# Optimization experiments

Hardware: AMD Instinct MI355X
Metric: run time of the kernel (lower is better)

Reference implementation:

```python
import jax, jax.numpy as jnp
import numpy as np

EPS_SLOPE = 1e-4
EPS_AVG = 1e-8
MIN_AVG = 1e-6
EPS_SCALE = 1e-3


def _slopes_yk(xk, delta_raw):
    # xk: [D, K] sorted knot x-positions; delta_raw: [D, K-1]
    seg_dx = xk[:, 1:] - xk[:, :-1]                      # [D, K-1]
    slopes = jax.nn.softplus(delta_raw) + EPS_SLOPE       # [D, K-1]
    avg = (slopes * seg_dx).sum(1, keepdims=True) / (seg_dx.sum(1, keepdims=True) + EPS_AVG)
    avg = jnp.maximum(avg, MIN_AVG)
    slopes = slopes / avg
    yk = jnp.concatenate(
        [jnp.zeros((xk.shape[0], 1), dtype=xk.dtype), jnp.cumsum(slopes * seg_dx, axis=1)],
        axis=1,
    )                                                     # [D, K]
    return slopes, yk


def setup_inputs() -> dict:
    key = jax.random.key(0)
    k1, k2, k3, k4, k5 = jax.random.split(key, 5)
    N, D, K = 1_000_000, 64, 32
    x = jax.random.normal(k1, (N, D), dtype=jnp.float32)
    # sorted knots per dim, spanning roughly the data range
    xk = jnp.sort(jax.random.normal(k2, (D, K), dtype=jnp.float32) * 2.0, axis=1)
    delta_raw = jax.random.normal(k3, (D, K - 1), dtype=jnp.float32) * 0.1
    scale_raw = jax.random.normal(k4, (D,), dtype=jnp.float32) * 0.1
    shift = jax.random.normal(k5, (D,), dtype=jnp.float32) * 0.1
    return {"x": x, "xk": xk, "delta_raw": delta_raw, "scale_raw": scale_raw, "shift": shift}


def reference(x, xk, delta_raw, scale_raw, shift):
    # x: [N, D]; xk: [D, K]
    D, K = xk.shape
    slopes, yk = _slopes_yk(xk, delta_raw)
    xT = x.T                                              # [D, N]
    # per-dim binary search (torch.searchsorted default == side='left')
    idx = jax.vmap(lambda knots, vals: jnp.searchsorted(knots, vals))(xk, xT)
    i0 = jnp.clip(idx, 1, K - 1) - 1                      # [D, N]
    x0 = jnp.take_along_axis(xk, i0, axis=1)              # [D, N]
    y0 = jnp.take_along_axis(yk, i0, axis=1)
    m = jnp.take_along_axis(slopes, i0, axis=1)
    y = (y0 + m * (xT - x0)).T                            # [N, D]
    scale = jax.nn.softplus(scale_raw) + EPS_SCALE
    return y * scale + shift
```

## Files before the change

kernel.cpp:

```cpp
#include <hip/hip_runtime.h>
#include <math.h>

#define D 64
#define KNOTS 32
#define NSEG 31
#define G 512
#define TPAD 516
#define SPAD 33

typedef float f4v __attribute__((ext_vector_type(4)));

__device__ __forceinline__ float softplus_f(float v) {
  return fmaxf(v, 0.f) + log1pf(expf(-fabsf(v)));
}

__global__ __launch_bounds__(512, 4) void pwl_fused(
    const float* __restrict__ x, const float* __restrict__ xk,
    const float* __restrict__ delta_raw, const float* __restrict__ scale_raw,
    const float* __restrict__ shift, float* __restrict__ out, int nrows) {
  __shared__ float kL[KNOTS * D];
  __shared__ float sA[D * SPAD];
  __shared__ float sB[D * SPAD];
  __shared__ unsigned char tab[D * TPAD];
  __shared__ float invS[D], nloS[D];

  const int tid = threadIdx.x;

  for (int i = tid; i < D * KNOTS; i += blockDim.x) {
    int d = i >> 5, j = i & 31;
    int sd = (d >> 2) | ((d & 3) << 4);
    kL[j * D + sd] = xk[i];
  }
  __syncthreads();

  if (tid < D) {
    const int sd = tid;
    const int d = ((sd & 15) << 2) | (sd >> 4);
    float num = 0.f, den = 0.f;
    for (int s = 0; s < NSEG; ++s) {
      float sp = softplus_f(delta_raw[d * NSEG + s]) + 1e-4f;
      float dx = kL[(s + 1) * D + sd] - kL[s * D + sd];
      num += sp * dx;
      den += dx;
    }
    float avg = fmaxf(num / (den + 1e-8f), 1e-6f);
    float scale = softplus_f(scale_raw[d]) + 1e-3f;
    float sh = shift[d];
    float y = 0.f;
    for (int s = 0; s < NSEG; ++s) {
      float sp = softplus_f(delta_raw[d * NSEG + s]) + 1e-4f;
      float m = sp / avg;
      float k0 = kL[s * D + sd];
      sA[sd * SPAD + s] = m * scale;
      sB[sd * SPAD + s] = (y - m * k0) * scale + sh;
      y += m * (kL[(s + 1) * D + sd] - k0);
    }
    float lo = kL[1 * D + sd];
    float hi = kL[(KNOTS - 1) * D + sd];
    float inv = (float)G / (hi - lo);
    invS[sd] = inv;
    nloS[sd] = -lo * inv;
  }
  __syncthreads();

  for (int p = tid; p < G * D; p += blockDim.x) {
    const int sd = p & 63;
    const int c = p >> 6;
    const float inv = invS[sd], nlo = nloS[sd];
    int b = 0;
#pragma unroll
    for (int half = 16; half > 0; half >>= 1) {
      float kv = kL[(b + half) * D + sd];
      float cf = fminf(fmaxf(fmaf(kv, inv, nlo), 0.f), (float)(G - 1));
      b += ((int)cf < c) ? half : 0;
    }
    tab[sd * TPAD + c] = (unsigned char)min(b, 30);
  }
  __syncthreads();

  const int lane = tid & 63;
  const int q = lane & 15;
  const int sd0 = q, sd1 = q + 16, sd2 = q + 32, sd3 = q + 48;
  const float inv0 = invS[sd0], nlo0 = nloS[sd0];
  const float inv1 = invS[sd1], nlo1 = nloS[sd1];
  const float inv2 = invS[sd2], nlo2 = nloS[sd2];
  const float inv3 = invS[sd3], nlo3 = nloS[sd3];

  const float* xp = x;
  float* op = out;
  const f4v* __restrict__ x4 = (const f4v*)x;
  f4v* __restrict__ o4 = (f4v*)out;

  auto evalquad = [&](f4v xv) -> f4v {
    float cf0 = fminf(fmaxf(fmaf(xv.x, inv0, nlo0), 0.f), (float)(G - 1));
    float cf1 = fminf(fmaxf(fmaf(xv.y, inv1, nlo1), 0.f), (float)(G - 1));
    float cf2 = fminf(fmaxf(fmaf(xv.z, inv2, nlo2), 0.f), (float)(G - 1));
    float cf3 = fminf(fmaxf(fmaf(xv.w, inv3, nlo3), 0.f), (float)(G - 1));
    int i0 = tab[sd0 * TPAD + (int)cf0];
    int i1 = tab[sd1 * TPAD + (int)cf1];
    int i2 = tab[sd2 * TPAD + (int)cf2];
    int i3 = tab[sd3 * TPAD + (int)cf3];
    f4v r;
    r.x = fmaf(sA[sd0 * SPAD + i0], xv.x, sB[sd0 * SPAD + i0]);
    r.y = fmaf(sA[sd1 * SPAD + i1], xv.y, sB[sd1 * SPAD + i1]);
    r.z = fmaf(sA[sd2 * SPAD + i2], xv.z, sB[sd2 * SPAD + i2]);
    r.w = fmaf(sA[sd3 * SPAD + i3], xv.w, sB[sd3 * SPAD + i3]);
    return r;
  };

  const int wid = (int)(blockIdx.x * blockDim.x + tid) >> 6;
  const int nw = (int)(gridDim.x * blockDim.x) >> 6;
  const int ngroups = nrows >> 4;
  const int chunk = (ngroups + nw - 1) / nw;
  int g0 = wid * chunk;
  const int gend = min(g0 + chunk, ngroups);
  const int navail = (gend > g0) ? (gend - g0) : 0;
  const int nfull = (navail / 3) * 3;

  f4v A0, A1, A2, A3, B0, B1, B2, B3, C0, C1, C2, C3;

#define GLOADI(bk, voff)                                                 \
  asm volatile("global_load_dwordx4 %0, %4, %5 offset:0\n\t"             \
               "global_load_dwordx4 %1, %4, %5 offset:1024\n\t"          \
               "global_load_dwordx4 %2, %4, %5 offset:2048\n\t"          \
               "global_load_dwordx4 %3, %4, %5 offset:3072"              \
               : "=&v"(bk##0), "=&v"(bk##1), "=&v"(bk##2), "=&v"(bk##3)  \
               : "v"(voff), "s"(xp))

#define WAITP(NSTR)                                              \
  asm volatile("s_waitcnt vmcnt(" NSTR ") expcnt(0)" ::: "memory"); \
  __builtin_amdgcn_sched_barrier(0)

#define STEP(bk, NSTR)                                                   \
  {                                                                      \
    WAITP(NSTR);                                                         \
    f4v r0_ = evalquad(bk##0);                                           \
    f4v r1_ = evalquad(bk##1);                                           \
    f4v r2_ = evalquad(bk##2);                                           \
    f4v r3_ = evalquad(bk##3);                                           \
    GLOADI(bk, voffN);                                                   \
    voffN = min(voffN + 4096u, maxL);                                    \
    asm volatile("global_store_dwordx4 %4, %0, %5 offset:0 nt\n\t"       \
                 "global_store_dwordx4 %4, %1, %5 offset:1024 nt\n\t"    \
                 "global_store_dwordx4 %4, %2, %5 offset:2048 nt\n\t"    \
                 "global_store_dwordx4 %4, %3, %5 offset:3072 nt"        \
                 :: "v"(r0_), "v"(r1_), "v"(r2_), "v"(r3_),              \
                    "v"(voffS), "s"(op));                                \
    voffS += 4096u;                                                      \
  }

  if (nfull >= 3) {
    const unsigned lb = (unsigned)lane * 16u;
    const unsigned maxL = (unsigned)(ngroups - 1) * 4096u + lb;
    unsigned voffS = (unsigned)g0 * 4096u + lb;
    unsigned voffN = voffS;
    GLOADI(A, voffN); voffN += 4096u;
    GLOADI(B, voffN); voffN += 4096u;
    GLOADI(C, voffN);
    voffN = min(voffN + 4096u, maxL);

    STEP(A, "8");
    STEP(B, "12");
    STEP(C, "16");
    const int trips3 = nfull / 3 - 1;
    for (int t = 0; t < trips3; ++t) {
      STEP(A, "20");
      STEP(B, "20");
      STEP(C, "20");
    }
    asm volatile("s_waitcnt vmcnt(0)" ::: "memory");
    __builtin_amdgcn_sched_barrier(0);
    g0 += nfull;
  }
#undef GLOADI
#undef WAITP
#undef STEP

  for (int g = g0; g < gend; ++g) {
    const int base = g * 256 + lane;
    f4v v0 = x4[base];
    f4v v1 = x4[base + 64];
    f4v v2 = x4[base + 128];
    f4v v3 = x4[base + 192];
    f4v r0 = evalquad(v0);
    f4v r1 = evalquad(v1);
    f4v r2 = evalquad(v2);
    f4v r3 = evalquad(v3);
    __builtin_nontemporal_store(r0, &o4[base]);
    __builtin_nontemporal_store(r1, &o4[base + 64]);
    __builtin_nontemporal_store(r2, &o4[base + 128]);
    __builtin_nontemporal_store(r3, &o4[base + 192]);
  }

  const int tr0 = ngroups << 4;
  for (int r = tr0 + wid; r < nrows; r += nw) {
    if (lane < 16) {
      const int bi = r * 16 + q;
      f4v xv = x4[bi];
      f4v rv = evalquad(xv);
      __builtin_nontemporal_store(rv, &o4[bi]);
    }
  }
}

extern "C" void kernel_launch(void* const* d_in, const int* in_sizes, int n_in,
                              void* d_out, int out_size, void* d_ws, size_t ws_size,
                              hipStream_t stream) {
  const float* x = (const float*)d_in[0];
  const float* xk = (const float*)d_in[1];
  const float* delta_raw = (const float*)d_in[2];
  const float* scale_raw = (const float*)d_in[3];
  const float* shift = (const float*)d_in[4];
  float* out = (float*)d_out;

  const int nrows = in_sizes[0] / D;
  const int block = 512;
  const int grid = 512;
  pwl_fused<<<grid, block, 0, stream>>>(x, xk, delta_raw, scale_raw, shift,
                                        out, nrows);
}
```

Baseline: 125.0 us.

## Shrink LDS lookup table and reuse knot storage to fit more blocks per CU

Measured after the change: 162.0 us. 1.3x slower.

```diff
diff --git a/kernel.cpp b/kernel.cpp
--- a/kernel.cpp
+++ b/kernel.cpp
@@ -4,9 +4,8 @@
 #define D 64
 #define KNOTS 32
 #define NSEG 31
-#define G 512
-#define TPAD 516
-#define SPAD 33
+#define G 384
+#define SPAD 32
 
 typedef float f4v __attribute__((ext_vector_type(4)));
 
@@ -21,8 +20,7 @@
   __shared__ float kL[KNOTS * D];
   __shared__ float sA[D * SPAD];
   __shared__ float sB[D * SPAD];
-  __shared__ unsigned char tab[D * TPAD];
-  __shared__ float invS[D], nloS[D];
+  __shared__ unsigned char tab[D * G];
 
   const int tid = threadIdx.x;
 
@@ -57,34 +55,43 @@
     }
     float lo = kL[1 * D + sd];
     float hi = kL[(KNOTS - 1) * D + sd];
-    float inv = (float)G / (hi - lo);
-    invS[sd] = inv;
-    nloS[sd] = -lo * inv;
+    kL[0 * D + sd] = (float)G / (hi - lo);
   }
   __syncthreads();
 
   for (int p = tid; p < G * D; p += blockDim.x) {
     const int sd = p & 63;
     const int c = p >> 6;
-    const float inv = invS[sd], nlo = nloS[sd];
+    const float lo = kL[1 * D + sd];
+    const float hi = kL[(KNOTS - 1) * D + sd];
+    const float w = (hi - lo) / (float)G;
+    const float xc = fmaf((float)c + 0.5f, w, lo);
     int b = 0;
 #pragma unroll
     for (int half = 16; half > 0; half >>= 1) {
-      float kv = kL[(b + half) * D + sd];
-      float cf = fminf(fmaxf(fmaf(kv, inv, nlo), 0.f), (float)(G - 1));
-      b += ((int)cf < c) ? half : 0;
-    }
-    tab[sd * TPAD + c] = (unsigned char)min(b, 30);
+      b += (kL[(b + half) * D + sd] < xc) ? half : 0;
+    }
+    int i0 = min(b, 30);
+    if (c == 0) i0 = 0;
+    if (c == G - 1) i0 = 30;
+    tab[sd * G + c] = (unsigned char)i0;
+  }
+  __syncthreads();
+
+  if (tid < D) {
+    float inv = kL[0 * D + tid];
+    float nlo = -kL[1 * D + tid] * inv;
+    kL[1 * D + tid] = nlo;
   }
   __syncthreads();
 
   const int lane = tid & 63;
   const int q = lane & 15;
   const int sd0 = q, sd1 = q + 16, sd2 = q + 32, sd3 = q + 48;
-  const float inv0 = invS[sd0], nlo0 = nloS[sd0];
-  const float inv1 = invS[sd1], nlo1 = nloS[sd1];
-  const float inv2 = invS[sd2], nlo2 = nloS[sd2];
-  const float inv3 = invS[sd3], nlo3 = nloS[sd3];
+  const float inv0 = kL[sd0], nlo0 = kL[D + sd0];
+  const float inv1 = kL[sd1], nlo1 = kL[D + sd1];
+  const float inv2 = kL[sd2], nlo2 = kL[D + sd2];
+  const float inv3 = kL[sd3], nlo3 = kL[D + sd3];
 
   const float* xp = x;
   float* op = out;
@@ -96,10 +103,10 @@
     float cf1 = fminf(fmaxf(fmaf(xv.y, inv1, nlo1), 0.f), (float)(G - 1));
     float cf2 = fminf(fmaxf(fmaf(xv.z, inv2, nlo2), 0.f), (float)(G - 1));
     float cf3 = fminf(fmaxf(fmaf(xv.w, inv3, nlo3), 0.f), (float)(G - 1));
-    int i0 = tab[sd0 * TPAD + (int)cf0];
-    int i1 = tab[sd1 * TPAD + (int)cf1];
-    int i2 = tab[sd2 * TPAD + (int)cf2];
-    int i3 = tab[sd3 * TPAD + (int)cf3];
+    int i0 = tab[sd0 * G + (int)cf0];
+    int i1 = tab[sd1 * G + (int)cf1];
+    int i2 = tab[sd2 * G + (int)cf2];
+    int i3 = tab[sd3 * G + (int)cf3];
     f4v r;
     r.x = fmaf(sA[sd0 * SPAD + i0], xv.x, sB[sd0 * SPAD + i0]);
     r.y = fmaf(sA[sd1 * SPAD + i1], xv.y, sB[sd1 * SPAD + i1]);
@@ -127,7 +134,7 @@
                : "=&v"(bk##0), "=&v"(bk##1), "=&v"(bk##2), "=&v"(bk##3)  \
                : "v"(voff), "s"(xp))
 
-#define WAITP(NSTR)                                              \
+#define WAITP(NSTR)                                                 \
   asm volatile("s_waitcnt vmcnt(" NSTR ") expcnt(0)" ::: "memory"); \
   __builtin_amdgcn_sched_barrier(0)
 
@@ -215,7 +222,7 @@
 
   const int nrows = in_sizes[0] / D;
   const int block = 512;
-  const int grid = 512;
+  const int grid = 768;
   pwl_fused<<<grid, block, 0, stream>>>(x, xk, delta_raw, scale_raw, shift,
                                         out, nrows);
 }
```
